# Kernel tuning notes

Hardware: AMD Instinct MI355X
Metric: run time of the kernel (lower is better)

Reference implementation:

```python
import jax, jax.numpy as jnp
import numpy as np

B, S, D, H, HD = 1, 4096, 1024, 16, 64
BLOCK = 128   # Fixed1/Fixed2 block_size (paper default for EnWik8)
C = 32        # Fixed2 'c' parameter
NEG = -1e10   # large negative bias for masked positions (flax make_attention_mask)


def build_sparse_mask(n: int) -> jnp.ndarray:
    """Merged Fixed1 + Fixed2 causal mask, shape [1,1,n,n] bool."""
    r = jnp.arange(n)
    q = r[:, None]
    k = r[None, :]
    lower = k <= q
    fixed1 = (q // BLOCK) == (k // BLOCK)
    rem = k % BLOCK
    fixed2 = (rem == 0) | (rem >= BLOCK - C)
    mask = lower & (fixed1 | fixed2)
    return mask[None, None, :, :]


def setup_inputs() -> dict:
    key = jax.random.key(0)
    ks = jax.random.split(key, 5)
    sc = 1.0 / np.sqrt(D)
    return {
        "x": jax.random.normal(ks[0], (B, S, D), jnp.float32),
        "Wq": jax.random.normal(ks[1], (D, H, HD), jnp.float32) * sc,
        "bq": jnp.zeros((H, HD), jnp.float32),
        "Wk": jax.random.normal(ks[2], (D, H, HD), jnp.float32) * sc,
        "bk": jnp.zeros((H, HD), jnp.float32),
        "Wv": jax.random.normal(ks[3], (D, H, HD), jnp.float32) * sc,
        "bv": jnp.zeros((H, HD), jnp.float32),
        "Wo": jax.random.normal(ks[4], (H, HD, D), jnp.float32) * (1.0 / np.sqrt(H * HD)),
        "bo": jnp.zeros((D,), jnp.float32),
    }


def reference(x, Wq, bq, Wk, bk, Wv, bv, Wo, bo):
    # QKV projections: [B,S,D] -> [B,S,H,HD]
    q = jnp.einsum("bsd,dhk->bshk", x, Wq) + bq
    k = jnp.einsum("bsd,dhk->bshk", x, Wk) + bk
    v = jnp.einsum("bsd,dhk->bshk", x, Wv) + bv

    bias = jnp.where(build_sparse_mask(S), 0.0, NEG).astype(x.dtype)

    # flax dot_product_attention: scale query, scores + bias, softmax, weighted sum
    q = q / jnp.sqrt(jnp.asarray(HD, x.dtype))
    scores = jnp.einsum("bqhd,bkhd->bhqk", q, k) + bias
    probs = jax.nn.softmax(scores, axis=-1)
    ctx = jnp.einsum("bhqk,bkhd->bqhd", probs, v)

    # output projection over (h, d) axes
    return jnp.einsum("bqhd,hdf->bqf", ctx, Wo) + bo
```

## Files before the change

kernel.cpp:

```cpp
#include <hip/hip_runtime.h>
#include <stdint.h>


#define S_LEN 4096
#define DMODEL 1024

typedef __bf16 bf16x8 __attribute__((ext_vector_type(8)));
typedef float  f32x4  __attribute__((ext_vector_type(4)));

__device__ __forceinline__ uint16_t f2bf(float f) {
    uint32_t u = __builtin_bit_cast(uint32_t, f);
    u += 0x7fffu + ((u >> 16) & 1u);
    return (uint16_t)(u >> 16);
}

__device__ __forceinline__ uint32_t pack2bf(float lo, float hi) {
    return (uint32_t)f2bf(lo) | ((uint32_t)f2bf(hi) << 16);
}

__device__ __forceinline__ void gload_lds16(const uint16_t* g, uint16_t* l) {
    __builtin_amdgcn_global_load_lds(
        (const __attribute__((address_space(1))) void*)g,
        (__attribute__((address_space(3))) void*)l, 16, 0, 0);
}

__device__ __forceinline__ int key_of(int b, int ngc, int ch, int kl) {
    if (ch >= ngc) return b * 128 + (ch - ngc) * 64 + kl;
    int t = ch * 64 + kl;
    int kb = t / 33, rr = t - kb * 33;
    return kb * 128 + (rr == 0 ? 0 : 95 + rr);
}

__global__ __launch_bounds__(256) void cvt_x_kernel(const float* __restrict__ x,
                                                    uint16_t* __restrict__ xb) {
    int i = (blockIdx.x * 256 + threadIdx.x) * 4;
    const float4 v = *(const float4*)(x + i);
    ushort4 o;
    o.x = f2bf(v.x); o.y = f2bf(v.y); o.z = f2bf(v.z); o.w = f2bf(v.w);
    *(ushort4*)(xb + i) = o;
}

__global__ __launch_bounds__(256) void tpose4(const float* __restrict__ Wq,
                                              const float* __restrict__ Wk,
                                              const float* __restrict__ Wv,
                                              const float* __restrict__ Wo,
                                              uint16_t* __restrict__ wqkvt,
                                              uint16_t* __restrict__ wot) {
    __shared__ float tile[64][65];
    const int z = blockIdx.z;
    const float* src = (z == 0) ? Wq : (z == 1) ? Wk : (z == 2) ? Wv : Wo;
    uint16_t* dst = (z < 3) ? (wqkvt + (size_t)z * 1024 * 1024) : wot;
    const int ro = blockIdx.y * 64, co = blockIdx.x * 64;
    const int c = threadIdx.x & 63, r4 = threadIdx.x >> 6;
#pragma unroll
    for (int i = 0; i < 16; i++) {
        int r = i * 4 + r4;
        tile[r][c] = src[(size_t)(ro + r) * 1024 + co + c];
    }
    __syncthreads();
#pragma unroll
    for (int i = 0; i < 16; i++) {
        int cc = i * 4 + r4;
        dst[(size_t)(co + cc) * 1024 + ro + c] = f2bf(tile[c][cc]);
    }
}

__global__ __launch_bounds__(256) void gemm_bt(const uint16_t* __restrict__ A,
                                               const uint16_t* __restrict__ Bt,
                                               const float* __restrict__ bias0,
                                               const float* __restrict__ bias1,
                                               const float* __restrict__ bias2,
                                               uint16_t* __restrict__ Cb,
                                               float* __restrict__ Cf,
                                               const int mode) {
    __shared__ __attribute__((aligned(16))) uint16_t As[128 * 64];
    __shared__ __attribute__((aligned(16))) uint16_t Bs[128 * 64];
    const int tid = threadIdx.x;
    const int wave = tid >> 6, lane = tid & 63;
    const int quad = lane >> 4, l16 = lane & 15;
    const int row0 = blockIdx.y * 128, col0 = blockIdx.x * 128;
    const int wm = (wave >> 1) * 64, wn = (wave & 1) * 64;
    const int srow = lane >> 3, scol = lane & 7;

    f32x4 acc[4][4];
    const f32x4 z4 = {0.f, 0.f, 0.f, 0.f};
#pragma unroll
    for (int i = 0; i < 4; i++)
#pragma unroll
        for (int j = 0; j < 4; j++) acc[i][j] = z4;

    for (int k0 = 0; k0 < 1024; k0 += 64) {
        __syncthreads();
#pragma unroll
        for (int i = 0; i < 4; i++) {
            int u = wave * 4 + i;
            int row = u * 8 + srow;
            gload_lds16(A  + (size_t)(row0 + row) * 1024 + k0 + scol * 8, As + u * 512);
            gload_lds16(Bt + (size_t)(col0 + row) * 1024 + k0 + scol * 8, Bs + u * 512);
        }
        __syncthreads();
#pragma unroll
        for (int kk = 0; kk < 2; kk++) {
            bf16x8 af[4], bfr[4];
#pragma unroll
            for (int mt = 0; mt < 4; mt++)
                af[mt] = *(const bf16x8*)(As + (wm + mt * 16 + l16) * 64 + kk * 32 + quad * 8);
#pragma unroll
            for (int nt = 0; nt < 4; nt++)
                bfr[nt] = *(const bf16x8*)(Bs + (wn + nt * 16 + l16) * 64 + kk * 32 + quad * 8);
#pragma unroll
            for (int mt = 0; mt < 4; mt++)
#pragma unroll
                for (int nt = 0; nt < 4; nt++)
                    acc[mt][nt] = __builtin_amdgcn_mfma_f32_16x16x32_bf16(
                        af[mt], bfr[nt], acc[mt][nt], 0, 0, 0);
        }
    }

    if (mode == 0) {
#pragma unroll
        for (int nt = 0; nt < 4; nt++) {
            int n = col0 + wn + nt * 16 + l16;
            int which = n >> 10, c = n & 1023;
            const float* bp = (which == 0) ? bias0 : (which == 1 ? bias1 : bias2);
            float bi = bp[c];
            float scv = (which == 0) ? 0.125f : 1.0f;
            uint16_t* op = Cb + (size_t)which * S_LEN * 1024 + c;
#pragma unroll
            for (int mt = 0; mt < 4; mt++) {
                int row = row0 + wm + mt * 16 + quad * 4;
#pragma unroll
                for (int r = 0; r < 4; r++)
                    op[(size_t)(row + r) * 1024] = f2bf((acc[mt][nt][r] + bi) * scv);
            }
        }
    } else {
#pragma unroll
        for (int nt = 0; nt < 4; nt++) {
            int n = col0 + wn + nt * 16 + l16;
            float bi = bias0[n];
#pragma unroll
            for (int mt = 0; mt < 4; mt++) {
                int row = row0 + wm + mt * 16 + quad * 4;
#pragma unroll
                for (int r = 0; r < 4; r++)
                    Cf[(size_t)(row + r) * 1024 + n] = acc[mt][nt][r] + bi;
            }
        }
    }
}

__global__ __launch_bounds__(512, 4) void attn_kernel(const uint16_t* __restrict__ Qg,
                                                      const uint16_t* __restrict__ Kg,
                                                      const uint16_t* __restrict__ Vg,
                                                      uint16_t* __restrict__ Og) {
    __shared__ __attribute__((aligned(16))) uint16_t SM[32768];
    uint16_t* Qs    = SM;
    uint16_t* Kbufs = SM + 8192;
    uint16_t* Vbufs = SM + 24576;

    const int h = blockIdx.y;
    const int b = (h < 8) ? (int)blockIdx.x : (31 - (int)blockIdx.x);
    const int tid = threadIdx.x;
    const int wave = tid >> 6, lane = tid & 63;
    const int quad = lane >> 4, l16 = lane & 15;
    const int grp = wave >> 2, wq = wave & 3;

    const int nprev = 33 * b;
    const int ngc = (nprev + 63) >> 6;
    const int ntot = ngc + 2;
    const int nit = (ntot + 1) >> 1;
    const size_t hoff = (size_t)h * 64;

    const int kRow = wave * 8 + (lane >> 3);
    const int kCol = (lane & 7) * 8;

#pragma unroll
    for (int i = 0; i < 2; i++) {
        int seg = i * 8 + wave;
        int row = seg * 8 + (lane >> 3);
        gload_lds16(Qg + (size_t)(b * 128 + row) * 1024 + hoff + kCol, Qs + seg * 512);
    }
#pragma unroll
    for (int g = 0; g < 2; g++) {
        if (g < ntot) {
            int key = key_of(b, ngc, g, kRow);
            gload_lds16(Kg + (size_t)key * 1024 + hoff + kCol,
                        Kbufs + g * 4096 + wave * 512);
        }
    }
    __syncthreads();

    float m_run[2], l_run[2];
    f32x4 o[4][2];
    const f32x4 z4 = {0.f, 0.f, 0.f, 0.f};
#pragma unroll
    for (int qt = 0; qt < 2; qt++) { m_run[qt] = -3e38f; l_run[qt] = 0.f; }
#pragma unroll
    for (int mt = 0; mt < 4; mt++) { o[mt][0] = z4; o[mt][1] = z4; }

    int cur = 0;
    for (int it = 0; it < nit; it++) {
        uint4 vreg[2];
#pragma unroll
        for (int g = 0; g < 2; g++) {
            int ch = 2 * it + g;
            if (ch < ntot) {
                int key = key_of(b, ngc, ch, lane);
                vreg[g] = *(const uint4*)(Vg + (size_t)key * 1024 + hoff + wave * 8);
            }
        }
#pragma unroll
        for (int g = 0; g < 2; g++) {
            int ch = 2 * (it + 1) + g;
            if (ch < ntot) {
                int key = key_of(b, ngc, ch, kRow);
                gload_lds16(Kg + (size_t)key * 1024 + hoff + kCol,
                            Kbufs + (cur ^ 1) * 8192 + g * 4096 + wave * 512);
            }
        }

        const int myc = 2 * it + grp;
        const bool have = (myc < ntot);
        uint32_t pk[4][2][2];
        float al[2] = {1.f, 1.f};
        if (have) {
            const uint16_t* Kc = Kbufs + cur * 8192 + grp * 4096;
            f32x4 s[4][2];
#pragma unroll
            for (int kt = 0; kt < 4; kt++) { s[kt][0] = z4; s[kt][1] = z4; }
#pragma unroll
            for (int kk = 0; kk < 2; kk++) {
                bf16x8 ka[4], qb[2];
#pragma unroll
                for (int kt = 0; kt < 4; kt++)
                    ka[kt] = *(const bf16x8*)(Kc + (kt * 16 + l16) * 64 + kk * 32 + quad * 8);
#pragma unroll
                for (int qt = 0; qt < 2; qt++)
                    qb[qt] = *(const bf16x8*)(Qs + (wq * 32 + qt * 16 + l16) * 64 + kk * 32 + quad * 8);
#pragma unroll
                for (int kt = 0; kt < 4; kt++)
#pragma unroll
                    for (int qt = 0; qt < 2; qt++)
                        s[kt][qt] = __builtin_amdgcn_mfma_f32_16x16x32_bf16(
                            ka[kt], qb[qt], s[kt][qt], 0, 0, 0);
            }
            if (myc >= ngc) {
                int cb = myc - ngc;
#pragma unroll
                for (int kt = 0; kt < 4; kt++) {
                    int keyl = cb * 64 + kt * 16 + quad * 4;
#pragma unroll
                    for (int qt = 0; qt < 2; qt++) {
                        int ql = wq * 32 + qt * 16 + l16;
#pragma unroll
                        for (int r = 0; r < 4; r++)
                            if (keyl + r > ql) s[kt][qt][r] = -1e30f;
                    }
                }
            } else if (myc == ngc - 1) {
#pragma unroll
                for (int kt = 0; kt < 4; kt++) {
                    int tg = myc * 64 + kt * 16 + quad * 4;
#pragma unroll
                    for (int r = 0; r < 4; r++)
                        if (tg + r >= nprev) {
                            s[kt][0][r] = -1e30f;
                            s[kt][1][r] = -1e30f;
                        }
                }
            }
#pragma unroll
            for (int qt = 0; qt < 2; qt++) {
                float mx = -3e38f;
#pragma unroll
                for (int kt = 0; kt < 4; kt++)
#pragma unroll
                    for (int r = 0; r < 4; r++) mx = fmaxf(mx, s[kt][qt][r]);
                mx = fmaxf(mx, __shfl_xor(mx, 16));
                mx = fmaxf(mx, __shfl_xor(mx, 32));
                float mn = fmaxf(m_run[qt], mx);
                float sub = fmaxf(mn, -1e20f);
                al[qt] = __expf(m_run[qt] - sub);
                m_run[qt] = mn;
                float ps = 0.f;
#pragma unroll
                for (int kt = 0; kt < 4; kt++) {
                    float p0 = __expf(s[kt][qt][0] - sub);
                    float p1 = __expf(s[kt][qt][1] - sub);
                    float p2 = __expf(s[kt][qt][2] - sub);
                    float p3 = __expf(s[kt][qt][3] - sub);
                    ps += (p0 + p1) + (p2 + p3);
                    pk[kt][qt][0] = pack2bf(p0, p1);
                    pk[kt][qt][1] = pack2bf(p2, p3);
                }
                ps += __shfl_xor(ps, 16);
                ps += __shfl_xor(ps, 32);
                l_run[qt] = l_run[qt] * al[qt] + ps;
            }
        }

#pragma unroll
        for (int g = 0; g < 2; g++) {
            int ch = 2 * it + g;
            if (ch < ntot) {
                uint16_t* Vd = Vbufs + g * 4096;
                uint32_t ww[4] = {vreg[g].x, vreg[g].y, vreg[g].z, vreg[g].w};
#pragma unroll
                for (int j = 0; j < 4; j++) {
                    Vd[(wave * 8 + 2 * j) * 64 + lane]     = (uint16_t)(ww[j] & 0xffffu);
                    Vd[(wave * 8 + 2 * j + 1) * 64 + lane] = (uint16_t)(ww[j] >> 16);
                }
            }
        }
        __syncthreads();

        if (have) {
            const uint16_t* Vc = Vbufs + grp * 4096;
#pragma unroll
            for (int mt = 0; mt < 4; mt++)
#pragma unroll
                for (int qt = 0; qt < 2; qt++)
#pragma unroll
                    for (int r = 0; r < 4; r++) o[mt][qt][r] *= al[qt];
            const int srcA = l16 + 32 * (quad & 1);
            const bool hi = (quad >> 1) != 0;
#pragma unroll
            for (int kk = 0; kk < 2; kk++) {
                bf16x8 va[4];
#pragma unroll
                for (int mt = 0; mt < 4; mt++)
                    va[mt] = *(const bf16x8*)(Vc + (mt * 16 + l16) * 64 + kk * 32 + quad * 8);
#pragma unroll
                for (int qt = 0; qt < 2; qt++) {
                    uint32_t u0a = (uint32_t)__shfl((int)pk[2 * kk][qt][0], srcA);
                    uint32_t u0b = (uint32_t)__shfl((int)pk[2 * kk + 1][qt][0], srcA);
                    uint32_t u1a = (uint32_t)__shfl((int)pk[2 * kk][qt][1], srcA);
                    uint32_t u1b = (uint32_t)__shfl((int)pk[2 * kk + 1][qt][1], srcA);
                    uint32_t u2a = (uint32_t)__shfl((int)pk[2 * kk][qt][0], srcA + 16);
                    uint32_t u2b = (uint32_t)__shfl((int)pk[2 * kk + 1][qt][0], srcA + 16);
                    uint32_t u3a = (uint32_t)__shfl((int)pk[2 * kk][qt][1], srcA + 16);
                    uint32_t u3b = (uint32_t)__shfl((int)pk[2 * kk + 1][qt][1], srcA + 16);
                    uint4 fr;
                    fr.x = hi ? u0b : u0a;
                    fr.y = hi ? u1b : u1a;
                    fr.z = hi ? u2b : u2a;
                    fr.w = hi ? u3b : u3a;
                    bf16x8 pb = __builtin_bit_cast(bf16x8, fr);
#pragma unroll
                    for (int mt = 0; mt < 4; mt++)
                        o[mt][qt] = __builtin_amdgcn_mfma_f32_16x16x32_bf16(
                            va[mt], pb, o[mt][qt], 0, 0, 0);
                }
            }
        }
        __syncthreads();
        cur ^= 1;
    }

    float* Obuf = (float*)(SM + 8192);
    float* mB = Obuf + 128 * 68;
    float* lB = mB + 128;
    if (grp == 1) {
#pragma unroll
        for (int qt = 0; qt < 2; qt++) {
            int ql = wq * 32 + qt * 16 + l16;
            if (quad == 0) { mB[ql] = m_run[qt]; lB[ql] = l_run[qt]; }
#pragma unroll
            for (int mt = 0; mt < 4; mt++)
                *(f32x4*)(Obuf + ql * 68 + mt * 16 + quad * 4) = o[mt][qt];
        }
    }
    __syncthreads();
    if (grp == 0) {
#pragma unroll
        for (int qt = 0; qt < 2; qt++) {
            int ql = wq * 32 + qt * 16 + l16;
            float mb = mB[ql], lb = lB[ql];
            float ms = fmaxf(m_run[qt], mb);
            float fa = __expf(m_run[qt] - ms);
            float fb = __expf(mb - ms);
            float inv = 1.0f / (l_run[qt] * fa + lb * fb);
            int q = b * 128 + ql;
#pragma unroll
            for (int mt = 0; mt < 4; mt++) {
                f32x4 ob = *(const f32x4*)(Obuf + ql * 68 + mt * 16 + quad * 4);
                ushort4 pko;
                pko.x = f2bf((o[mt][qt][0] * fa + ob[0] * fb) * inv);
                pko.y = f2bf((o[mt][qt][1] * fa + ob[1] * fb) * inv);
                pko.z = f2bf((o[mt][qt][2] * fa + ob[2] * fb) * inv);
                pko.w = f2bf((o[mt][qt][3] * fa + ob[3] * fb) * inv);
                *(ushort4*)(Og + (size_t)q * 1024 + hoff + mt * 16 + quad * 4) = pko;
            }
        }
    }
}

extern "C" void kernel_launch(void* const* d_in, const int* in_sizes, int n_in,
                              void* d_out, int out_size, void* d_ws, size_t ws_size,
                              hipStream_t stream) {
    const float* x  = (const float*)d_in[0];
    const float* Wq = (const float*)d_in[1];
    const float* bq = (const float*)d_in[2];
    const float* Wk = (const float*)d_in[3];
    const float* bk = (const float*)d_in[4];
    const float* Wv = (const float*)d_in[5];
    const float* bv = (const float*)d_in[6];
    const float* Wo = (const float*)d_in[7];
    const float* bo = (const float*)d_in[8];
    float* out = (float*)d_out;

    uint8_t* ws = (uint8_t*)d_ws;
    uint16_t* x_bf  = (uint16_t*)(ws);
    uint16_t* wqkvt = (uint16_t*)(ws + (8u << 20));
    uint16_t* wot   = (uint16_t*)(ws + (14u << 20));
    uint16_t* q_bf  = (uint16_t*)(ws + (16u << 20));
    uint16_t* k_bf  = (uint16_t*)(ws + (24u << 20));
    uint16_t* v_bf  = (uint16_t*)(ws + (32u << 20));
    uint16_t* ctx   = (uint16_t*)(ws + (40u << 20));
    if (ws_size < (48u << 20)) return;

    cvt_x_kernel<<<4096, 256, 0, stream>>>(x, x_bf);
    tpose4<<<dim3(16, 16, 4), 256, 0, stream>>>(Wq, Wk, Wv, Wo, wqkvt, wot);
    gemm_bt<<<dim3(24, 32), 256, 0, stream>>>(x_bf, wqkvt, bq, bk, bv,
                                              q_bf, nullptr, 0);
    attn_kernel<<<dim3(32, 16), 512, 0, stream>>>(q_bf, k_bf, v_bf, ctx);
    gemm_bt<<<dim3(8, 32), 256, 0, stream>>>(ctx, wot, bo, nullptr, nullptr,
                                             nullptr, out, 1);
}
```

Measured before the change: 212.8 us.

## XOR-swizzle LDS tiles and vectorize QKV GEMM epilogue via swapped MFMA operands

Applies an XOR swizzle to the 16-byte column chunks of the A/B tiles in the GEMM and of the Q/K/V tiles in the attention kernel, so that row-strided ds_read_b128 fragment loads stop hitting the same LDS banks. In the QKV projection GEMM the MFMA operands are swapped so each lane holds four consecutive output columns. That lets the epilogue load bias as a float4 and write packed 8-byte bf16 stores instead of scattered 2-byte stores. The V transpose writes into LDS also follow the swizzled layout, at the cost of extra index arithmetic.

```diff
diff --git a/kernel.cpp b/kernel.cpp
--- a/kernel.cpp
+++ b/kernel.cpp
@@ -65,14 +65,14 @@
     }
 }
 
+template <int MODE>
 __global__ __launch_bounds__(256) void gemm_bt(const uint16_t* __restrict__ A,
                                                const uint16_t* __restrict__ Bt,
                                                const float* __restrict__ bias0,
                                                const float* __restrict__ bias1,
                                                const float* __restrict__ bias2,
                                                uint16_t* __restrict__ Cb,
-                                               float* __restrict__ Cf,
-                                               const int mode) {
+                                               float* __restrict__ Cf) {
     __shared__ __attribute__((aligned(16))) uint16_t As[128 * 64];
     __shared__ __attribute__((aligned(16))) uint16_t Bs[128 * 64];
     const int tid = threadIdx.x;
@@ -81,6 +81,8 @@
     const int row0 = blockIdx.y * 128, col0 = blockIdx.x * 128;
     const int wm = (wave >> 1) * 64, wn = (wave & 1) * 64;
     const int srow = lane >> 3, scol = lane & 7;
+    const int gcol = (scol ^ srow) * 8;
+    const int sw = (l16 & 7);
 
     f32x4 acc[4][4];
     const f32x4 z4 = {0.f, 0.f, 0.f, 0.f};
@@ -95,8 +97,8 @@
         for (int i = 0; i < 4; i++) {
             int u = wave * 4 + i;
             int row = u * 8 + srow;
-            gload_lds16(A  + (size_t)(row0 + row) * 1024 + k0 + scol * 8, As + u * 512);
-            gload_lds16(Bt + (size_t)(col0 + row) * 1024 + k0 + scol * 8, Bs + u * 512);
+            gload_lds16(A  + (size_t)(row0 + row) * 1024 + k0 + gcol, As + u * 512);
+            gload_lds16(Bt + (size_t)(col0 + row) * 1024 + k0 + gcol, Bs + u * 512);
         }
         __syncthreads();
 #pragma unroll
@@ -104,34 +106,42 @@
             bf16x8 af[4], bfr[4];
 #pragma unroll
             for (int mt = 0; mt < 4; mt++)
-                af[mt] = *(const bf16x8*)(As + (wm + mt * 16 + l16) * 64 + kk * 32 + quad * 8);
+                af[mt] = *(const bf16x8*)(As + (wm + mt * 16 + l16) * 64 + ((kk * 4 + quad) ^ sw) * 8);
 #pragma unroll
             for (int nt = 0; nt < 4; nt++)
-                bfr[nt] = *(const bf16x8*)(Bs + (wn + nt * 16 + l16) * 64 + kk * 32 + quad * 8);
+                bfr[nt] = *(const bf16x8*)(Bs + (wn + nt * 16 + l16) * 64 + ((kk * 4 + quad) ^ sw) * 8);
 #pragma unroll
             for (int mt = 0; mt < 4; mt++)
 #pragma unroll
-                for (int nt = 0; nt < 4; nt++)
-                    acc[mt][nt] = __builtin_amdgcn_mfma_f32_16x16x32_bf16(
-                        af[mt], bfr[nt], acc[mt][nt], 0, 0, 0);
-        }
-    }
-
-    if (mode == 0) {
+                for (int nt = 0; nt < 4; nt++) {
+                    if (MODE == 0)
+                        acc[mt][nt] = __builtin_amdgcn_mfma_f32_16x16x32_bf16(
+                            bfr[nt], af[mt], acc[mt][nt], 0, 0, 0);
+                    else
+                        acc[mt][nt] = __builtin_amdgcn_mfma_f32_16x16x32_bf16(
+                            af[mt], bfr[nt], acc[mt][nt], 0, 0, 0);
+                }
+        }
+    }
+
+    if (MODE == 0) {
 #pragma unroll
         for (int nt = 0; nt < 4; nt++) {
-            int n = col0 + wn + nt * 16 + l16;
+            int n = col0 + wn + nt * 16 + quad * 4;
             int which = n >> 10, c = n & 1023;
             const float* bp = (which == 0) ? bias0 : (which == 1 ? bias1 : bias2);
-            float bi = bp[c];
+            const float4 b4 = *(const float4*)(bp + c);
             float scv = (which == 0) ? 0.125f : 1.0f;
             uint16_t* op = Cb + (size_t)which * S_LEN * 1024 + c;
 #pragma unroll
             for (int mt = 0; mt < 4; mt++) {
-                int row = row0 + wm + mt * 16 + quad * 4;
-#pragma unroll
-                for (int r = 0; r < 4; r++)
-                    op[(size_t)(row + r) * 1024] = f2bf((acc[mt][nt][r] + bi) * scv);
+                int s = row0 + wm + mt * 16 + l16;
+                ushort4 pkv;
+                pkv.x = f2bf((acc[mt][nt][0] + b4.x) * scv);
+                pkv.y = f2bf((acc[mt][nt][1] + b4.y) * scv);
+                pkv.z = f2bf((acc[mt][nt][2] + b4.z) * scv);
+                pkv.w = f2bf((acc[mt][nt][3] + b4.w) * scv);
+                *(ushort4*)(op + (size_t)s * 1024) = pkv;
             }
         }
     } else {
@@ -165,6 +175,7 @@
     const int wave = tid >> 6, lane = tid & 63;
     const int quad = lane >> 4, l16 = lane & 15;
     const int grp = wave >> 2, wq = wave & 3;
+    const int sw = (l16 & 7);
 
     const int nprev = 33 * b;
     const int ngc = (nprev + 63) >> 6;
@@ -173,19 +184,19 @@
     const size_t hoff = (size_t)h * 64;
 
     const int kRow = wave * 8 + (lane >> 3);
-    const int kCol = (lane & 7) * 8;
+    const int gCol = ((lane & 7) ^ (lane >> 3)) * 8;
 
 #pragma unroll
     for (int i = 0; i < 2; i++) {
         int seg = i * 8 + wave;
         int row = seg * 8 + (lane >> 3);
-        gload_lds16(Qg + (size_t)(b * 128 + row) * 1024 + hoff + kCol, Qs + seg * 512);
+        gload_lds16(Qg + (size_t)(b * 128 + row) * 1024 + hoff + gCol, Qs + seg * 512);
     }
 #pragma unroll
     for (int g = 0; g < 2; g++) {
         if (g < ntot) {
             int key = key_of(b, ngc, g, kRow);
-            gload_lds16(Kg + (size_t)key * 1024 + hoff + kCol,
+            gload_lds16(Kg + (size_t)key * 1024 + hoff + gCol,
                         Kbufs + g * 4096 + wave * 512);
         }
     }
@@ -215,7 +226,7 @@
             int ch = 2 * (it + 1) + g;
             if (ch < ntot) {
                 int key = key_of(b, ngc, ch, kRow);
-                gload_lds16(Kg + (size_t)key * 1024 + hoff + kCol,
+                gload_lds16(Kg + (size_t)key * 1024 + hoff + gCol,
                             Kbufs + (cur ^ 1) * 8192 + g * 4096 + wave * 512);
             }
         }
@@ -234,10 +245,10 @@
                 bf16x8 ka[4], qb[2];
 #pragma unroll
                 for (int kt = 0; kt < 4; kt++)
-                    ka[kt] = *(const bf16x8*)(Kc + (kt * 16 + l16) * 64 + kk * 32 + quad * 8);
+                    ka[kt] = *(const bf16x8*)(Kc + (kt * 16 + l16) * 64 + ((kk * 4 + quad) ^ sw) * 8);
 #pragma unroll
                 for (int qt = 0; qt < 2; qt++)
-                    qb[qt] = *(const bf16x8*)(Qs + (wq * 32 + qt * 16 + l16) * 64 + kk * 32 + quad * 8);
+                    qb[qt] = *(const bf16x8*)(Qs + (wq * 32 + qt * 16 + l16) * 64 + ((kk * 4 + quad) ^ sw) * 8);
 #pragma unroll
                 for (int kt = 0; kt < 4; kt++)
 #pragma unroll
@@ -306,10 +317,12 @@
             if (ch < ntot) {
                 uint16_t* Vd = Vbufs + g * 4096;
                 uint32_t ww[4] = {vreg[g].x, vreg[g].y, vreg[g].z, vreg[g].w};
+                const int kc = (lane >> 3), kin = (lane & 7);
 #pragma unroll
                 for (int j = 0; j < 4; j++) {
-                    Vd[(wave * 8 + 2 * j) * 64 + lane]     = (uint16_t)(ww[j] & 0xffffu);
-                    Vd[(wave * 8 + 2 * j + 1) * 64 + lane] = (uint16_t)(ww[j] >> 16);
+                    int hd0 = wave * 8 + 2 * j, hd1 = hd0 + 1;
+                    Vd[hd0 * 64 + ((kc ^ (hd0 & 7)) * 8 + kin)] = (uint16_t)(ww[j] & 0xffffu);
+                    Vd[hd1 * 64 + ((kc ^ (hd1 & 7)) * 8 + kin)] = (uint16_t)(ww[j] >> 16);
                 }
             }
         }
@@ -330,7 +343,7 @@
                 bf16x8 va[4];
 #pragma unroll
                 for (int mt = 0; mt < 4; mt++)
-                    va[mt] = *(const bf16x8*)(Vc + (mt * 16 + l16) * 64 + kk * 32 + quad * 8);
+                    va[mt] = *(const bf16x8*)(Vc + (mt * 16 + l16) * 64 + ((kk * 4 + quad) ^ sw) * 8);
 #pragma unroll
                 for (int qt = 0; qt < 2; qt++) {
                     uint32_t u0a = (uint32_t)__shfl((int)pk[2 * kk][qt][0], srcA);
@@ -422,9 +435,9 @@
 
     cvt_x_kernel<<<4096, 256, 0, stream>>>(x, x_bf);
     tpose4<<<dim3(16, 16, 4), 256, 0, stream>>>(Wq, Wk, Wv, Wo, wqkvt, wot);
-    gemm_bt<<<dim3(24, 32), 256, 0, stream>>>(x_bf, wqkvt, bq, bk, bv,
-                                              q_bf, nullptr, 0);
+    gemm_bt<0><<<dim3(24, 32), 256, 0, stream>>>(x_bf, wqkvt, bq, bk, bv,
+                                                 q_bf, nullptr);
     attn_kernel<<<dim3(32, 16), 512, 0, stream>>>(q_bf, k_bf, v_bf, ctx);
-    gemm_bt<<<dim3(8, 32), 256, 0, stream>>>(ctx, wot, bo, nullptr, nullptr,
-                                             nullptr, out, 1);
-}
+    gemm_bt<1><<<dim3(8, 32), 256, 0, stream>>>(ctx, wot, bo, nullptr, nullptr,
+                                                nullptr, out);
+}
```

Result: faster. 196.9 us (-7.5%).
